# Performance work log

Hardware: AMD Instinct MI355X
Metric: run time of the kernel (lower is better)

## Reference

```python
import jax, jax.numpy as jnp
from jax import lax
import numpy as np

RADIUS = 15
EPSILON = 0.001
DN = ('NCHW', 'OIHW', 'NCHW')


def conv2d(x, w, b, pad):
    y = lax.conv_general_dilated(x, w, (1, 1), [(pad, pad), (pad, pad)],
                                 dimension_numbers=DN)
    return y + b[None, :, None, None]


def box_filter(x, radius):
    # Equivalent to zero-padded 2D (2r+1)x(2r+1) averaging conv, done separably.
    k = 2 * radius + 1
    B, C, H, W = x.shape
    xr = x.reshape(B * C, 1, H, W)
    kh = jnp.ones((1, 1, k, 1), x.dtype) / k
    kw = jnp.ones((1, 1, 1, k), x.dtype) / k
    y = lax.conv_general_dilated(xr, kh, (1, 1), [(radius, radius), (0, 0)],
                                 dimension_numbers=DN)
    y = lax.conv_general_dilated(y, kw, (1, 1), [(0, 0), (radius, radius)],
                                 dimension_numbers=DN)
    return y.reshape(B, C, H, W)


def guided_filter(I, p, radius, epsilon):
    mean_I = box_filter(I, radius)
    mean_p = box_filter(p, radius)
    mean_Ip = box_filter(I * p, radius)
    cov_Ip = mean_Ip - mean_I * mean_p
    mean_II = box_filter(I * I, radius)
    var_I = mean_II - mean_I * mean_I
    a = cov_Ip / (var_I + epsilon)
    b = mean_p - a * mean_I
    mean_a = box_filter(a, radius)
    mean_b = box_filter(b, radius)
    return mean_a * I + mean_b


def setup_inputs() -> dict:
    key = jax.random.key(0)
    ks = jax.random.split(key, 10)
    B, H, W = 8, 512, 512
    I = jax.random.uniform(ks[0], (B, 3, H, W), dtype=jnp.float32)
    t_initial = jax.random.uniform(ks[1], (B, 1, H, W), dtype=jnp.float32)
    dark_channel = jax.random.uniform(ks[2], (B, H, W), dtype=jnp.float32)
    A = jax.random.uniform(ks[3], (B, 3), dtype=jnp.float32)
    # refine_net params (first conv takes the 8-channel concat: 3+1+1+3)
    W1 = jax.random.normal(ks[4], (32, 8, 3, 3), jnp.float32) * 0.05
    b1 = jnp.zeros((32,), jnp.float32)
    W2 = jax.random.normal(ks[5], (16, 32, 3, 3), jnp.float32) * 0.05
    b2 = jnp.zeros((16,), jnp.float32)
    W3 = jax.random.normal(ks[6], (1, 16, 3, 3), jnp.float32) * 0.05
    b3 = jnp.zeros((1,), jnp.float32)
    return {"I": I, "t_initial": t_initial, "dark_channel": dark_channel,
            "A": A, "W1": W1, "b1": b1, "W2": W2, "b2": b2,
            "W3": W3, "b3": b3}


def reference(I, t_initial, dark_channel, A, W1, b1, W2, b2, W3, b3):
    B, C, H, W = I.shape
    # luma
    I_gray = 0.299 * I[:, 0:1] + 0.587 * I[:, 1:2] + 0.114 * I[:, 2:3]
    t_guided = guided_filter(I_gray, t_initial, RADIUS, EPSILON)
    dark_expanded = dark_channel[:, None]                    # [B,1,H,W]
    A_expanded = jnp.broadcast_to(A[:, :, None, None], (B, 3, H, W))
    feats = jnp.concatenate([I, t_guided, dark_expanded, A_expanded], axis=1)
    h = jax.nn.relu(conv2d(feats, W1, b1, 1))
    h = jax.nn.relu(conv2d(h, W2, b2, 1))
    t_refined = jax.nn.sigmoid(conv2d(h, W3, b3, 1))
    t_final = 0.7 * t_guided + 0.3 * t_refined
    return jnp.clip(t_final, 0.0, 1.0)
```

## Files before the change

kernel.cpp:

```cpp
#include <hip/hip_runtime.h>
#include <cmath>

#define BB 8
#define HH 512
#define WW 512
#define HW (HH*WW)
#define RAD 15
#define SEG 16
#define EPS 0.001f
#define INV_K (1.0f/31.0f)
#define TROWS 16
#define NPX 272
#define XOFF (-8)

typedef _Float16 h16x8 __attribute__((ext_vector_type(8)));
typedef _Float16 h16x4 __attribute__((ext_vector_type(4)));
typedef _Float16 h16x2 __attribute__((ext_vector_type(2)));
typedef float f32x4 __attribute__((ext_vector_type(4)));
typedef float f32x2 __attribute__((ext_vector_type(2)));
typedef int   i32x4 __attribute__((ext_vector_type(4)));

static __device__ inline int s3(int r) { return (r + 6) % 3; }


__global__ __launch_bounds__(256) void k_gray_hbox4(const float* __restrict__ I,
                                                    const float* __restrict__ p,
                                                    const float* __restrict__ dark,
                                                    float* __restrict__ g,
                                                    h16x4* __restrict__ hq,
                                                    _Float16* __restrict__ feats,
                                                    const float* __restrict__ W1,
                                                    const float* __restrict__ W2,
                                                    _Float16* __restrict__ wf1,
                                                    _Float16* __restrict__ wf2) {
    __shared__ float sg[WW], sp[WW];
    int row = blockIdx.x;
    int b = row >> 9;
    int base = row * WW;
    const float* Ib = I + (size_t)b * 3 * HW + (size_t)(row & 511) * WW;
    const float* db = dark + (size_t)base;
    int tid = threadIdx.x;
    for (int x = tid; x < WW; x += 256) {
        float i0 = Ib[x], i1 = Ib[HW + x], i2 = Ib[2 * HW + x];
        float gv = 0.299f * i0 + 0.587f * i1 + 0.114f * i2;
        sg[x] = gv; sp[x] = p[base + x];
        g[base + x] = gv;
        h16x4 v;
        v[0] = (_Float16)i0; v[1] = (_Float16)i1; v[2] = (_Float16)i2;
        v[3] = (_Float16)db[x];
        *(h16x4*)(feats + ((size_t)base + x) * 8) = v;
    }
    __syncthreads();
    for (int x = tid; x < WW; x += 256) {
        float s0 = 0.f, s1 = 0.f, s2 = 0.f, s3v = 0.f;
        int lo = x - RAD < 0 ? 0 : x - RAD;
        int hi = x + RAD >= WW ? WW - 1 : x + RAD;
        for (int i = lo; i <= hi; ++i) {
            float gv = sg[i], pv = sp[i];
            s0 += gv; s1 += pv; s2 += gv * pv; s3v += gv * gv;
        }
        h16x4 o;
        o[0] = (_Float16)(s0 * INV_K); o[1] = (_Float16)(s1 * INV_K);
        o[2] = (_Float16)(s2 * INV_K); o[3] = (_Float16)(s3v * INV_K);
        hq[base + x] = o;
    }
    if (blockIdx.x == 0 && tid < 64) {
        int lane = tid;
        int j = lane & 15, gg = lane >> 4;
        const int cmap[8] = {0, 1, 2, 4, 3, 5, 6, 7};
#pragma unroll
        for (int cg = 0; cg < 2; ++cg)
#pragma unroll
            for (int t = 0; t < 3; ++t) {
                int s = t * 4 + gg;
                h16x8 w;
#pragma unroll
                for (int i = 0; i < 8; ++i)
                    w[i] = (s < 9) ? (_Float16)W1[(cg * 16 + j) * 72 + cmap[i] * 9 + s]
                                   : (_Float16)0.f;
                *(h16x8*)(wf1 + ((cg * 3 + t) * 64 + lane) * 8) = w;
            }
        int ci0 = gg * 8;
#pragma unroll
        for (int s = 0; s < 9; ++s) {
            h16x8 w;
#pragma unroll
            for (int i = 0; i < 8; ++i)
                w[i] = (_Float16)W2[j * 288 + (ci0 + i) * 9 + s];
            *(h16x8*)(wf2 + (s * 64 + lane) * 8) = w;
        }
    }
}

__global__ __launch_bounds__(256) void k_vbox4_ab(const h16x4* __restrict__ hq,
                                                  h16x2* __restrict__ ab) {
    int x = blockIdx.x * 256 + threadIdx.x;
    int b = blockIdx.y;
    int y0 = blockIdx.z * SEG;
    int pbase = b * HW + x;
    f32x4 s = { 0.f, 0.f, 0.f, 0.f };
    int r0 = y0 - RAD < 0 ? 0 : y0 - RAD;
    for (int r = r0; r < y0 + RAD; ++r) {
        h16x4 v = hq[pbase + r * WW];
        s[0] += (float)v[0]; s[1] += (float)v[1]; s[2] += (float)v[2]; s[3] += (float)v[3];
    }
    for (int y = y0; y < y0 + SEG; ++y) {
        if (y + RAD < HH) {
            h16x4 v = hq[pbase + (y + RAD) * WW];
            s[0] += (float)v[0]; s[1] += (float)v[1]; s[2] += (float)v[2]; s[3] += (float)v[3];
        }
        float mI = s[0] * INV_K, mP = s[1] * INV_K, mIp = s[2] * INV_K, mII = s[3] * INV_K;
        float cov = mIp - mI * mP;
        float var = mII - mI * mI;
        float av = cov / (var + EPS);
        float bv = mP - av * mI;
        h16x2 o;
        o[0] = (_Float16)av; o[1] = (_Float16)bv;
        ab[pbase + y * WW] = o;
        if (y - RAD >= 0) {
            h16x4 v = hq[pbase + (y - RAD) * WW];
            s[0] -= (float)v[0]; s[1] -= (float)v[1]; s[2] -= (float)v[2]; s[3] -= (float)v[3];
        }
    }
}

__global__ __launch_bounds__(256) void k_hbox2(const h16x2* __restrict__ ab,
                                               h16x2* __restrict__ hab) {
    __shared__ float sa[WW], sb[WW];
    int base = blockIdx.x * WW;
    int tid = threadIdx.x;
    for (int x = tid; x < WW; x += 256) {
        h16x2 v = ab[base + x];
        sa[x] = (float)v[0]; sb[x] = (float)v[1];
    }
    __syncthreads();
    for (int x = tid; x < WW; x += 256) {
        float s0 = 0.f, s1 = 0.f;
        int lo = x - RAD < 0 ? 0 : x - RAD;
        int hi = x + RAD >= WW ? WW - 1 : x + RAD;
        for (int i = lo; i <= hi; ++i) { s0 += sa[i]; s1 += sb[i]; }
        h16x2 o;
        o[0] = (_Float16)(s0 * INV_K); o[1] = (_Float16)(s1 * INV_K);
        hab[base + x] = o;
    }
}

__global__ __launch_bounds__(256) void k_vbox2_tg(const h16x2* __restrict__ hab,
                                                  const float* __restrict__ g,
                                                  const float* __restrict__ A,
                                                  float* __restrict__ tg,
                                                  _Float16* __restrict__ feats) {
    int x = blockIdx.x * 256 + threadIdx.x;
    int b = blockIdx.y;
    int y0 = blockIdx.z * SEG;
    int pbase = b * HW + x;
    _Float16 A0 = (_Float16)A[b * 3 + 0], A1 = (_Float16)A[b * 3 + 1], A2 = (_Float16)A[b * 3 + 2];
    f32x2 s = { 0.f, 0.f };
    int r0 = y0 - RAD < 0 ? 0 : y0 - RAD;
    for (int r = r0; r < y0 + RAD; ++r) {
        h16x2 v = hab[pbase + r * WW];
        s[0] += (float)v[0]; s[1] += (float)v[1];
    }
    for (int y = y0; y < y0 + SEG; ++y) {
        if (y + RAD < HH) {
            h16x2 v = hab[pbase + (y + RAD) * WW];
            s[0] += (float)v[0]; s[1] += (float)v[1];
        }
        int o = pbase + y * WW;
        float val = (s[0] * INV_K) * g[o] + (s[1] * INV_K);
        tg[o] = val;
        h16x4 fv;
        fv[0] = (_Float16)val; fv[1] = A0; fv[2] = A1; fv[3] = A2;
        *(h16x4*)(feats + (size_t)o * 8 + 4) = fv;
        if (y - RAD >= 0) {
            h16x2 v = hab[pbase + (y - RAD) * WW];
            s[0] -= (float)v[0]; s[1] -= (float)v[1];
        }
    }
}

static __device__ inline h16x8 ld_h1(const _Float16* hrow, int lp, int c) {
    int sp = c ^ ((lp >> 1) & 3);
    return *(const h16x8*)(hrow + lp * 32 + sp * 8);
}
static __device__ inline void st_h1(_Float16* hrow, int lp, int u, h16x4 o) {
    int sp = (u >> 1) ^ ((lp >> 1) & 3);
    *(h16x4*)(hrow + lp * 32 + sp * 8 + (u & 1) * 4) = o;
}
static __device__ inline void st_h2(_Float16* hrow, int lp, int u, h16x4 o) {
    int sp = (u >> 1) ^ ((lp >> 2) & 1);
    *(h16x4*)(hrow + lp * 16 + sp * 8 + (u & 1) * 4) = o;
}

static __device__ inline void load_b1(const _Float16* fb, int r1, int X0, int g,
                                      int j, int gq, h16x8 Bg[3]) {
    const h16x8 z = {0,0,0,0,0,0,0,0};
    bool xedgeG = (X0 == 0 && g == 0) || (X0 == 256 && g == 16);
    int gxb = X0 + XOFF + g * 16 + j;
    if (!xedgeG && r1 >= 1 && r1 <= 509) {
#pragma unroll
        for (int t = 0; t < 3; ++t) {
            int s = t * 4 + gq;
            int dy = s / 3 - 1, dx = s - (s / 3) * 3 - 1;
            Bg[t] = *(const h16x8*)(fb + ((size_t)(r1 + dy) * WW + (gxb + dx)) * 8);
        }
    } else {
#pragma unroll
        for (int t = 0; t < 3; ++t) {
            int s = t * 4 + gq;
            int dy = s / 3 - 1, dx = s - (s / 3) * 3 - 1;
            int yy = r1 + dy, xx = gxb + dx;
            bool ok = (s < 9) && yy >= 0 && yy < HH && xx >= 0 && xx < WW;
            int yc = yy < 0 ? 0 : (yy > HH - 1 ? HH - 1 : yy);
            int xc = xx < 0 ? 0 : (xx > WW - 1 ? WW - 1 : xx);
            h16x8 v = *(const h16x8*)(fb + ((size_t)yc * WW + xc) * 8);
            Bg[t] = ok ? v : z;
        }
    }
}

__global__ __launch_bounds__(512, 2) void k_cnn_fused(const _Float16* __restrict__ feats,
                                                      const _Float16* __restrict__ wf1,
                                                      const _Float16* __restrict__ wf2,
                                                      const float* __restrict__ b1,
                                                      const float* __restrict__ b2,
                                                      const float* __restrict__ W3,
                                                      const float* __restrict__ b3,
                                                      const float* __restrict__ tg,
                                                      float* __restrict__ out) {
    __shared__ _Float16 h1s[3][NPX * 32];
    __shared__ _Float16 h2s2[2][NPX * 16];
    __shared__ h16x8 wf1s[6 * 64];
    __shared__ h16x2 w3s[72];
    __shared__ float sB[48];
    __shared__ float w3bias;

    int tid = threadIdx.x;
    int lane = tid & 63, wave = tid >> 6;
    int j = lane & 15, gq = lane >> 4;
    int b = blockIdx.y;
    int X0 = (blockIdx.x & 1) * 256;
    int y0 = (blockIdx.x >> 1) * TROWS;
    const _Float16* fb = feats + (size_t)b * HW * 8;
    const float* tgb = tg + (size_t)b * HW;
    float* outb = out + (size_t)b * HW;

    for (int q = tid; q < 384; q += 512)
        ((i32x4*)wf1s)[q] = ((const i32x4*)wf1)[q];
    const h16x8* wf2v = (const h16x8*)wf2;
    h16x8 wA2[9];
#pragma unroll
    for (int s = 0; s < 9; ++s) wA2[s] = wf2v[s * 64 + lane];
    if (tid < 72) {
        int s = tid >> 3, u = tid & 7;
        h16x2 w;
        w[0] = (_Float16)W3[(2 * u) * 9 + s];
        w[1] = (_Float16)W3[(2 * u + 1) * 9 + s];
        w3s[tid] = w;
    } else if (tid < 104) {
        sB[tid - 72] = b1[tid - 72];
    } else if (tid < 120) {
        sB[32 + tid - 104] = b2[tid - 104];
    } else if (tid == 120) w3bias = b3[0];
    __syncthreads();

    int g0 = wave * 2;
    const h16x8 z16 = {0,0,0,0,0,0,0,0};
    h16x8 Bv[2][3];
    h16x8 Bg[3];
    f32x4 cA[2] = {}, cB[2] = {}, cC[2] = {};
    f32x4 gA = {}, gB = {}, gC = {};
    int c3px = tid >> 1, c3h = tid & 1;
    float accN = 0.f, accC3 = 0.f;

    for (int i = 0; i < TROWS + 6; ++i) {
        int r1 = y0 + i - 2;
        int rp = y0 + i - 3;
        int r2 = y0 + i - 4;
        int R  = y0 + i - 5;
        bool do_h1 = (i <= TROWS + 3) && (r1 >= 0) && (r1 <= 511);
        bool do_rp = (i >= 1) && (i <= TROWS + 4) && (rp >= 0) && (rp <= 511);
        bool st_r2 = (i <= TROWS + 4) && (r2 >= 0) && (r2 <= 511);
        bool rd_R  = (R >= 0) && (R <= 511);

        if (do_h1) {
#pragma unroll
            for (int k = 0; k < 2; ++k)
                load_b1(fb, r1, X0, g0 + k, j, gq, Bv[k]);
            if (wave == 5) load_b1(fb, r1, X0, 16, j, gq, Bg);
        }
        float tgv = 0.f;
        int oOut = (y0 + i - 6) * WW + X0 + c3px;
        if (i >= 6 && c3h == 0) tgv = tgb[oOut];

        f32x4 bias2v = *(const f32x4*)(sB + 32 + gq * 4);
#pragma unroll
        for (int k = 0; k < 2; ++k) {
            cA[k] = cB[k]; cB[k] = cC[k]; cC[k] = bias2v;
        }
        if (wave == 4) { gA = gB; gB = gC; gC = bias2v; }
        if (do_rp) {
            const _Float16* hrow = h1s[s3(rp)];
#pragma unroll
            for (int k = 0; k < 2; ++k) {
                int lpb = (g0 + k) * 16 + j;
#pragma unroll
                for (int dx = 0; dx < 3; ++dx) {
                    int lpx = lpb + dx - 1;
                    h16x8 v;
                    if (wave == 0 && k == 0) {
                        int lpc = lpx < 0 ? 0 : lpx;
                        v = ld_h1(hrow, lpc, gq);
                        if (X0 == 0) v = (lpx >= 8) ? v : z16;
                    } else {
                        v = ld_h1(hrow, lpx, gq);
                    }
                    cC[k] = __builtin_amdgcn_mfma_f32_16x16x32_f16(wA2[0 + dx], v, cC[k], 0, 0, 0);
                    cB[k] = __builtin_amdgcn_mfma_f32_16x16x32_f16(wA2[3 + dx], v, cB[k], 0, 0, 0);
                    cA[k] = __builtin_amdgcn_mfma_f32_16x16x32_f16(wA2[6 + dx], v, cA[k], 0, 0, 0);
                }
            }
            if (wave == 4) {
                int lpb = 256 + j;
#pragma unroll
                for (int dx = 0; dx < 3; ++dx) {
                    int lpx = lpb + dx - 1;
                    int lpc = lpx > NPX - 1 ? NPX - 1 : lpx;
                    h16x8 v = ld_h1(hrow, lpc, gq);
                    if (X0 == 256 && lpx > 263) v = z16;
                    gC = __builtin_amdgcn_mfma_f32_16x16x32_f16(wA2[0 + dx], v, gC, 0, 0, 0);
                    gB = __builtin_amdgcn_mfma_f32_16x16x32_f16(wA2[3 + dx], v, gB, 0, 0, 0);
                    gA = __builtin_amdgcn_mfma_f32_16x16x32_f16(wA2[6 + dx], v, gA, 0, 0, 0);
                }
            }
        }

        if (st_r2) {
            _Float16* h2row = h2s2[r2 & 1];
#pragma unroll
            for (int k = 0; k < 2; ++k) {
                h16x4 o;
#pragma unroll
                for (int r = 0; r < 4; ++r) o[r] = (_Float16)fmaxf(cA[k][r], 0.f);
                st_h2(h2row, (g0 + k) * 16 + j, gq, o);
            }
            if (wave == 4) {
                h16x4 o;
#pragma unroll
                for (int r = 0; r < 4; ++r) o[r] = (_Float16)fmaxf(gA[r], 0.f);
                st_h2(h2row, 256 + j, gq, o);
            }
        }

        {
            float d0 = 0.f, d1 = 0.f, d2 = 0.f;
            if (rd_R) {
                const _Float16* hrow = h2s2[R & 1];
#pragma unroll
                for (int dx = 0; dx < 3; ++dx) {
                    int xim = X0 + c3px + dx - 1;
                    if (xim >= 0 && xim < WW) {
                        int lpx = c3px + 8 + dx - 1;
                        int sp = c3h ^ ((lpx >> 2) & 1);
                        h16x8 v = *(const h16x8*)(hrow + lpx * 16 + sp * 8);
#pragma unroll
                        for (int q = 0; q < 4; ++q) {
                            h16x2 pv = { v[2 * q], v[2 * q + 1] };
                            d0 = __builtin_amdgcn_fdot2(pv, w3s[(0 + dx) * 8 + 4 * c3h + q], d0, false);
                            d1 = __builtin_amdgcn_fdot2(pv, w3s[(3 + dx) * 8 + 4 * c3h + q], d1, false);
                            d2 = __builtin_amdgcn_fdot2(pv, w3s[(6 + dx) * 8 + 4 * c3h + q], d2, false);
                        }
                    }
                }
            }
            if (i >= 6) {
                float accv = accC3 + d2;
                float full = accv + __shfl_xor(accv, 1) + w3bias;
                if (c3h == 0) {
                    float sg = 1.f / (1.f + expf(-full));
                    float tf = 0.7f * tgv + 0.3f * sg;
                    outb[oOut] = fminf(fmaxf(tf, 0.f), 1.f);
                }
            }
            accC3 = accN + d1;
            accN = d0;
        }

        if (do_h1) {
            h16x8 w1[2][3];
#pragma unroll
            for (int cg = 0; cg < 2; ++cg)
#pragma unroll
                for (int t = 0; t < 3; ++t) w1[cg][t] = wf1s[(cg * 3 + t) * 64 + lane];
            _Float16* h1row = h1s[s3(r1)];
            f32x4 b1lo = *(const f32x4*)(sB + gq * 4);
            f32x4 b1hi = *(const f32x4*)(sB + 16 + gq * 4);
#pragma unroll
            for (int k = 0; k < 2; ++k) {
                f32x4 a1[2] = { b1lo, b1hi };
#pragma unroll
                for (int t = 0; t < 3; ++t)
#pragma unroll
                    for (int cg = 0; cg < 2; ++cg)
                        a1[cg] = __builtin_amdgcn_mfma_f32_16x16x32_f16(w1[cg][t], Bv[k][t], a1[cg], 0, 0, 0);
                int lp = (g0 + k) * 16 + j;
#pragma unroll
                for (int cg = 0; cg < 2; ++cg) {
                    h16x4 o;
#pragma unroll
                    for (int r = 0; r < 4; ++r) o[r] = (_Float16)fmaxf(a1[cg][r], 0.f);
                    st_h1(h1row, lp, cg * 4 + gq, o);
                }
            }
            if (wave == 5) {
                f32x4 a1[2] = { b1lo, b1hi };
#pragma unroll
                for (int t = 0; t < 3; ++t)
#pragma unroll
                    for (int cg = 0; cg < 2; ++cg)
                        a1[cg] = __builtin_amdgcn_mfma_f32_16x16x32_f16(w1[cg][t], Bg[t], a1[cg], 0, 0, 0);
                int lp = 256 + j;
#pragma unroll
                for (int cg = 0; cg < 2; ++cg) {
                    h16x4 o;
#pragma unroll
                    for (int r = 0; r < 4; ++r) o[r] = (_Float16)fmaxf(a1[cg][r], 0.f);
                    st_h1(h1row, lp, cg * 4 + gq, o);
                }
            }
        }
        __syncthreads();
    }
}

extern "C" void kernel_launch(void* const* d_in, const int* in_sizes, int n_in,
                              void* d_out, int out_size, void* d_ws, size_t ws_size,
                              hipStream_t stream) {
    const float* I    = (const float*)d_in[0];
    const float* t0   = (const float*)d_in[1];
    const float* dark = (const float*)d_in[2];
    const float* A    = (const float*)d_in[3];
    const float* W1   = (const float*)d_in[4];
    const float* b1   = (const float*)d_in[5];
    const float* W2   = (const float*)d_in[6];
    const float* b2   = (const float*)d_in[7];
    const float* W3   = (const float*)d_in[8];
    const float* b3   = (const float*)d_in[9];
    float* out = (float*)d_out;
    float* ws  = (float*)d_ws;

    const size_t P = (size_t)BB * HW;
    float* tg       = ws;
    _Float16* feats = (_Float16*)(ws + P);
    float* g        = ws + 5 * P;
    h16x4* hq       = (h16x4*)(ws + 6 * P);
    h16x2* ab       = (h16x2*)(ws + 8 * P);
    h16x2* hab      = (h16x2*)(ws + 9 * P);
    _Float16* wf1   = (_Float16*)(ws + 10 * P);
    _Float16* wf2   = wf1 + 6 * 64 * 8;

    k_gray_hbox4<<<BB * HH, 256, 0, stream>>>(I, t0, dark, g, hq, feats, W1, W2, wf1, wf2);
    dim3 gv(WW / 256, BB, HH / SEG);
    k_vbox4_ab<<<gv, 256, 0, stream>>>(hq, ab);
    k_hbox2<<<BB * HH, 256, 0, stream>>>(ab, hab);
    k_vbox2_tg<<<gv, 256, 0, stream>>>(hab, g, A, tg, feats);

    dim3 gf(64, BB);
    k_cnn_fused<<<gf, 512, 0, stream>>>(feats, wf1, wf2, b1, b2, W3, b3, tg, out);
}
```

Baseline: 181.2 us.

## Fuse vertical box of four stats with horizontal box of a,b

Merges the vertical running-sum kernel that computes a and b with the following horizontal box filter kernel. Each block now covers half a row width plus a 15-pixel halo (271 columns) and computes a and b in shared memory per row. Each block then applies the horizontal 31-tap sum directly, so the intermediate ab buffer and one launch are removed. In exchange, halo columns are computed twice, there is a __syncthreads per output row, and only 2x8x32 blocks are launched, which may underfill the GPU.

```diff
diff --git a/kernel.cpp b/kernel.cpp
--- a/kernel.cpp
+++ b/kernel.cpp
@@ -12,6 +12,7 @@
 #define TROWS 16
 #define NPX 272
 #define XOFF (-8)
+#define NCOL 271
 
 typedef _Float16 h16x8 __attribute__((ext_vector_type(8)));
 typedef _Float16 h16x4 __attribute__((ext_vector_type(4)));
@@ -92,56 +93,73 @@
     }
 }
 
-__global__ __launch_bounds__(256) void k_vbox4_ab(const h16x4* __restrict__ hq,
-                                                  h16x2* __restrict__ ab) {
-    int x = blockIdx.x * 256 + threadIdx.x;
+__global__ __launch_bounds__(256) void k_vhbox(const h16x4* __restrict__ hq,
+                                               h16x2* __restrict__ hab) {
+    __shared__ float sa[2][NCOL + 1], sb[2][NCOL + 1];
+    int tid = threadIdx.x;
+    int X0 = blockIdx.x * 256;
     int b = blockIdx.y;
     int y0 = blockIdx.z * SEG;
-    int pbase = b * HW + x;
-    f32x4 s = { 0.f, 0.f, 0.f, 0.f };
+    int xa0 = (X0 == 0) ? 0 : (WW - NCOL);
+    int pbase = b * HW;
+
+    int c0 = xa0 + tid;
+    int c1 = xa0 + 256 + tid;
+    bool has2 = (tid < NCOL - 256);
+
+    f32x4 s0 = {0.f, 0.f, 0.f, 0.f}, s1 = {0.f, 0.f, 0.f, 0.f};
     int r0 = y0 - RAD < 0 ? 0 : y0 - RAD;
     for (int r = r0; r < y0 + RAD; ++r) {
-        h16x4 v = hq[pbase + r * WW];
-        s[0] += (float)v[0]; s[1] += (float)v[1]; s[2] += (float)v[2]; s[3] += (float)v[3];
+        h16x4 v = hq[pbase + r * WW + c0];
+        s0[0] += (float)v[0]; s0[1] += (float)v[1]; s0[2] += (float)v[2]; s0[3] += (float)v[3];
+        if (has2) {
+            h16x4 w = hq[pbase + r * WW + c1];
+            s1[0] += (float)w[0]; s1[1] += (float)w[1]; s1[2] += (float)w[2]; s1[3] += (float)w[3];
+        }
     }
     for (int y = y0; y < y0 + SEG; ++y) {
         if (y + RAD < HH) {
-            h16x4 v = hq[pbase + (y + RAD) * WW];
-            s[0] += (float)v[0]; s[1] += (float)v[1]; s[2] += (float)v[2]; s[3] += (float)v[3];
-        }
-        float mI = s[0] * INV_K, mP = s[1] * INV_K, mIp = s[2] * INV_K, mII = s[3] * INV_K;
-        float cov = mIp - mI * mP;
-        float var = mII - mI * mI;
-        float av = cov / (var + EPS);
-        float bv = mP - av * mI;
+            h16x4 v = hq[pbase + (y + RAD) * WW + c0];
+            s0[0] += (float)v[0]; s0[1] += (float)v[1]; s0[2] += (float)v[2]; s0[3] += (float)v[3];
+            if (has2) {
+                h16x4 w = hq[pbase + (y + RAD) * WW + c1];
+                s1[0] += (float)w[0]; s1[1] += (float)w[1]; s1[2] += (float)w[2]; s1[3] += (float)w[3];
+            }
+        }
+        int buf = y & 1;
+        {
+            float mI = s0[0] * INV_K, mP = s0[1] * INV_K, mIp = s0[2] * INV_K, mII = s0[3] * INV_K;
+            float cov = mIp - mI * mP;
+            float var = mII - mI * mI;
+            float av = cov / (var + EPS);
+            sa[buf][tid] = av;
+            sb[buf][tid] = mP - av * mI;
+        }
+        if (has2) {
+            float mI = s1[0] * INV_K, mP = s1[1] * INV_K, mIp = s1[2] * INV_K, mII = s1[3] * INV_K;
+            float cov = mIp - mI * mP;
+            float var = mII - mI * mI;
+            float av = cov / (var + EPS);
+            sa[buf][256 + tid] = av;
+            sb[buf][256 + tid] = mP - av * mI;
+        }
+        __syncthreads();
+        int x = X0 + tid;
+        int lo = (x - RAD < 0 ? 0 : x - RAD) - xa0;
+        int hi = (x + RAD > WW - 1 ? WW - 1 : x + RAD) - xa0;
+        float ha = 0.f, hb = 0.f;
+        for (int i = lo; i <= hi; ++i) { ha += sa[buf][i]; hb += sb[buf][i]; }
         h16x2 o;
-        o[0] = (_Float16)av; o[1] = (_Float16)bv;
-        ab[pbase + y * WW] = o;
+        o[0] = (_Float16)(ha * INV_K); o[1] = (_Float16)(hb * INV_K);
+        hab[pbase + y * WW + x] = o;
         if (y - RAD >= 0) {
-            h16x4 v = hq[pbase + (y - RAD) * WW];
-            s[0] -= (float)v[0]; s[1] -= (float)v[1]; s[2] -= (float)v[2]; s[3] -= (float)v[3];
-        }
-    }
-}
-
-__global__ __launch_bounds__(256) void k_hbox2(const h16x2* __restrict__ ab,
-                                               h16x2* __restrict__ hab) {
-    __shared__ float sa[WW], sb[WW];
-    int base = blockIdx.x * WW;
-    int tid = threadIdx.x;
-    for (int x = tid; x < WW; x += 256) {
-        h16x2 v = ab[base + x];
-        sa[x] = (float)v[0]; sb[x] = (float)v[1];
-    }
-    __syncthreads();
-    for (int x = tid; x < WW; x += 256) {
-        float s0 = 0.f, s1 = 0.f;
-        int lo = x - RAD < 0 ? 0 : x - RAD;
-        int hi = x + RAD >= WW ? WW - 1 : x + RAD;
-        for (int i = lo; i <= hi; ++i) { s0 += sa[i]; s1 += sb[i]; }
-        h16x2 o;
-        o[0] = (_Float16)(s0 * INV_K); o[1] = (_Float16)(s1 * INV_K);
-        hab[base + x] = o;
+            h16x4 v = hq[pbase + (y - RAD) * WW + c0];
+            s0[0] -= (float)v[0]; s0[1] -= (float)v[1]; s0[2] -= (float)v[2]; s0[3] -= (float)v[3];
+            if (has2) {
+                h16x4 w = hq[pbase + (y - RAD) * WW + c1];
+                s1[0] -= (float)w[0]; s1[1] -= (float)w[1]; s1[2] -= (float)w[2]; s1[3] -= (float)w[3];
+            }
+        }
     }
 }
 
@@ -454,16 +472,14 @@
     _Float16* feats = (_Float16*)(ws + P);
     float* g        = ws + 5 * P;
     h16x4* hq       = (h16x4*)(ws + 6 * P);
-    h16x2* ab       = (h16x2*)(ws + 8 * P);
-    h16x2* hab      = (h16x2*)(ws + 9 * P);
-    _Float16* wf1   = (_Float16*)(ws + 10 * P);
+    h16x2* hab      = (h16x2*)(ws + 8 * P);
+    _Float16* wf1   = (_Float16*)(ws + 9 * P);
     _Float16* wf2   = wf1 + 6 * 64 * 8;
 
     k_gray_hbox4<<<BB * HH, 256, 0, stream>>>(I, t0, dark, g, hq, feats, W1, W2, wf1, wf2);
-    dim3 gv(WW / 256, BB, HH / SEG);
-    k_vbox4_ab<<<gv, 256, 0, stream>>>(hq, ab);
-    k_hbox2<<<BB * HH, 256, 0, stream>>>(ab, hab);
-    k_vbox2_tg<<<gv, 256, 0, stream>>>(hab, g, A, tg, feats);
+    dim3 gb(2, BB, HH / SEG);
+    k_vhbox<<<gb, 256, 0, stream>>>(hq, hab);
+    k_vbox2_tg<<<gb, 256, 0, stream>>>(hab, g, A, tg, feats);
 
     dim3 gf(64, BB);
     k_cnn_fused<<<gf, 512, 0, stream>>>(feats, wf1, wf2, b1, b2, W3, b3, tg, out);
```

Result: slower. 193.9 us (+7.0%).
